# Kernel optimization log

Hardware: AMD Instinct MI355X
Metric: run time of the kernel (lower is better)

The kernel has to match this reference:

```python
import jax, jax.numpy as jnp
import numpy as np
from jax import lax

S = 30      # num_sensors
FD = 200    # feature_dim
T = 1024    # signal length
B = 1024    # batch
NC = 7      # num_classes


def setup_inputs() -> dict:
    key = jax.random.key(0)
    ks = jax.random.split(key, 24)
    rn = lambda i, shape: jax.random.normal(ks[i], shape, jnp.float32) * 0.05
    # normalized adjacency with self-loops: D^-1/2 (A+I) D^-1/2
    rng = np.random.default_rng(0)
    A = (rng.random((S, S)) > 0.7).astype(np.float32)
    A = ((A + A.T) > 0).astype(np.float32)
    A_self = A + np.eye(S, dtype=np.float32)
    dinv = 1.0 / np.sqrt(A_self.sum(1))
    adj_self = jnp.asarray(dinv[:, None] * A_self * dinv[None, :])
    return dict(
        x=jax.random.normal(ks[0], (B, S, T), jnp.float32),
        adj_self=adj_self,
        Wc1=rn(1, (S, S, 3)), bc1=jnp.zeros((S,), jnp.float32),
        Wc2=rn(2, (S, S, 3)), bc2=jnp.zeros((S,), jnp.float32),
        Wt=rn(3, (T, FD)), bt=jnp.zeros((FD,), jnp.float32),
        Wa=rn(4, (FD, FD)),
        Wm1=rn(5, (FD, FD)), Wm2=rn(6, (FD, FD)), Wm3=rn(7, (FD, FD)),
        Wg1=rn(8, (FD, FD)), Wg2=rn(9, (FD, FD)),
        wg=rn(10, (FD, 3)),
        Wp1=rn(11, (FD, FD // 2)), Wp2=rn(12, (FD, FD // 2)), Wp3=rn(13, (FD, FD // 2)),
        Wl=rn(14, (FD, 150)), Wgl=rn(15, (FD, 150)),
        Ws1=rn(16, (S, S // 2)), Ws2=rn(17, (S // 2, S)),
        Wf1=rn(18, (300, 150)), Wf2=rn(19, (150, 300)),
        Wcls=rn(20, (S * 600, NC)), bcls=jnp.zeros((NC,), jnp.float32),
    )


def reference(x, adj_self, Wc1, bc1, Wc2, bc2, Wt, bt, Wa, Wm1, Wm2, Wm3,
              Wg1, Wg2, wg, Wp1, Wp2, Wp3, Wl, Wgl, Ws1, Ws2, Wf1, Wf2,
              Wcls, bcls):
    dn = ('NCH', 'OIH', 'NCH')
    # CNN feature extractor: [B,S,T] -> [B,S,FD]
    h = jax.nn.relu(lax.conv_general_dilated(x, Wc1, (1,), 'SAME', dimension_numbers=dn) + bc1[None, :, None])
    h = jax.nn.relu(lax.conv_general_dilated(h, Wc2, (1,), 'SAME', dimension_numbers=dn) + bc2[None, :, None])
    F2 = jax.nn.relu(jnp.einsum('bst,tf->bsf', h, Wt) + bt)
    # MGCN: learned feature adjacency + 3-order GCN (batched, replaces per-sample loop)
    A_F = jax.nn.softmax(jax.nn.relu(jnp.einsum('bif,fg,bjg->bij', F2, Wa, F2)), axis=-1)
    gc = lambda A, X, W: jax.nn.relu(jnp.einsum('bij,bjf,fg->big', A, X, W))
    x1 = gc(A_F, F2, Wm1)
    x2 = gc(A_F, x1, Wm2)
    x3 = gc(A_F, x2, Wm3)
    # signal GCN on physical adjacency (2-layer, eval mode so dropout is identity)
    h1 = jax.nn.relu(jnp.einsum('ij,bjf,fg->big', adj_self, F2, Wg1))
    x_sensor = jnp.einsum('ij,bjf,fg->big', adj_self, h1, Wg2)
    H1 = (x1 + x_sensor) * 0.5
    H2 = (x2 + x_sensor) * 0.5
    H3 = (x3 + x_sensor) * 0.5
    # adaptive aggregation: per-node softmax gate over 3 branches, project to FD//2 each -> 300
    scores = jnp.stack([jnp.einsum('bsf,f->bs', H, wg[:, k]) for k, H in enumerate((H1, H2, H3))], -1)
    g = jax.nn.softmax(scores, -1)  # [B,S,3]
    agg = lambda k, H, Wp: jnp.einsum('ij,bjf,fg->big', adj_self, g[..., k:k + 1] * H, Wp)
    G_h = jnp.concatenate([agg(0, H1, Wp1), agg(1, H2, Wp2), agg(2, H3, Wp3)], -1)  # [B,S,300]
    # LGFM: local (physical adj) + global (learned adj) -> 150+150
    loc = jax.nn.relu(jnp.einsum('ij,bjf,fg->big', adj_self, F2, Wl))
    glb = jax.nn.relu(jnp.einsum('bij,bjf,fg->big', A_F, F2, Wgl))
    G_v = jnp.concatenate([loc, glb], -1)  # [B,S,300]
    # cross squeeze-excitation: channel SE on G_h driven by G_v, feature SE on G_v driven by G_h
    wch = jax.nn.sigmoid(jax.nn.relu(G_v.mean(-1) @ Ws1) @ Ws2)   # [B,S]
    G_h_att = G_h * wch[:, :, None]
    wft = jax.nn.sigmoid(jax.nn.relu(G_h.mean(1) @ Wf1) @ Wf2)    # [B,300]
    G_v_att = G_v * wft[:, None, :]
    G = jnp.concatenate([G_h_att, G_v_att], -1).reshape(x.shape[0], -1)  # [B, S*600]
    return jax.nn.log_softmax(G @ Wcls + bcls, axis=-1)
```

## Files before the change

kernel.cpp:

```cpp
#include <hip/hip_runtime.h>
#include <math.h>

#define S   30
#define FD  200
#define TT  1024
#define BB  1024
#define NC  7

#define OFS_C1   0ull
#define OFS_F2   31457280ull
#define OFS_AF   0ull
#define OFS_GV   921600ull
#define OFS_GH   10137600ull
#define OFS_WCH  19353600ull
#define OFS_WFT  19384320ull
#define OFS_R    19691520ull

__global__ __launch_bounds__(256) void k_conv1(
    const float* __restrict__ x,
    const float* __restrict__ Wc1, const float* __restrict__ bc1,
    float* __restrict__ C1) {
    const int c = blockIdx.x, b = blockIdx.y;
    const int t = threadIdx.x;
    const int t0 = c * 256;
    __shared__ float xb[S * 258];
    __shared__ float w1l[90 * 32];
    for (int idx = t; idx < 2700; idx += 256) {
        int so = idx / 90, r = idx % 90;
        w1l[r * 32 + so] = Wc1[idx];
    }
    for (int idx = t; idx < 180; idx += 256) {
        int r = idx >> 1, z = idx & 1;
        w1l[r * 32 + 30 + z] = 0.f;
    }
    for (int idx = t; idx < S * 64; idx += 256) {
        int s = idx >> 6, u = idx & 63;
        float4 v = *(const float4*)(x + (size_t)(b * S + s) * TT + t0 + 4 * u);
        float* d = xb + s * 258 + 1 + 4 * u;
        d[0] = v.x; d[1] = v.y; d[2] = v.z; d[3] = v.w;
    }
    if (t < 60) {
        int s = t % S;
        if (t < S) {
            int gt = t0 - 1;
            xb[s * 258] = (gt >= 0) ? x[(size_t)(b * S + s) * TT + gt] : 0.f;
        } else {
            int gt = t0 + 256;
            xb[s * 258 + 257] = (gt < TT) ? x[(size_t)(b * S + s) * TT + gt] : 0.f;
        }
    }
    __syncthreads();
    float acc[32];
#pragma unroll
    for (int so = 0; so < 32; so++) acc[so] = (so < S) ? bc1[so] : 0.f;
    for (int si = 0; si < S; si++) {
        float v0 = xb[si * 258 + t];
        float v1 = xb[si * 258 + t + 1];
        float v2 = xb[si * 258 + t + 2];
        const float* wr = w1l + si * 96;
#pragma unroll
        for (int u = 0; u < 8; u++) {
            float4 w0 = *(const float4*)(wr + 4 * u);
            float4 w1 = *(const float4*)(wr + 32 + 4 * u);
            float4 w2 = *(const float4*)(wr + 64 + 4 * u);
            acc[4 * u + 0] = fmaf(w0.x, v0, fmaf(w1.x, v1, fmaf(w2.x, v2, acc[4 * u + 0])));
            acc[4 * u + 1] = fmaf(w0.y, v0, fmaf(w1.y, v1, fmaf(w2.y, v2, acc[4 * u + 1])));
            acc[4 * u + 2] = fmaf(w0.z, v0, fmaf(w1.z, v1, fmaf(w2.z, v2, acc[4 * u + 2])));
            acc[4 * u + 3] = fmaf(w0.w, v0, fmaf(w1.w, v1, fmaf(w2.w, v2, acc[4 * u + 3])));
        }
    }
#pragma unroll
    for (int so = 0; so < 32; so++) {
        if (so < S)
            C1[(size_t)(b * S + so) * TT + t0 + t] = fmaxf(acc[so], 0.f);
    }
}

#define FMA4(av, wv, accm)                           \
    {                                                \
        accm[0] = fmaf(av, (wv).x, accm[0]);         \
        accm[1] = fmaf(av, (wv).y, accm[1]);         \
        accm[2] = fmaf(av, (wv).z, accm[2]);         \
        accm[3] = fmaf(av, (wv).w, accm[3]);         \
    }

__device__ inline void fma_tile8(const float4 a0, const float4 a1,
                                 const float4 w[8], float accm[4]) {
    FMA4(a0.x, w[0], accm); FMA4(a0.y, w[1], accm);
    FMA4(a0.z, w[2], accm); FMA4(a0.w, w[3], accm);
    FMA4(a1.x, w[4], accm); FMA4(a1.y, w[5], accm);
    FMA4(a1.z, w[6], accm); FMA4(a1.w, w[7], accm);
}

template<int RPT>
__device__ inline void zacc(float acc[][4]) {
#pragma unroll
    for (int m = 0; m < RPT; m++)
#pragma unroll
        for (int q = 0; q < 4; q++) acc[m][q] = 0.f;
}

template<int RPT, int N, int K>
__device__ inline void gemm_w4_pf(const float* Xl, int xstr, const float* __restrict__ W,
                                  int ct, int rt, float acc[][4]) {
    const float* wp = W + 4 * ct;
    float4 wreg[8];
#pragma unroll
    for (int u = 0; u < 8; u++) wreg[u] = *(const float4*)(wp + u * N);
#pragma unroll 1
    for (int kt = 0; kt < K / 8 - 1; kt++) {
        float4 wnxt[8];
#pragma unroll
        for (int u = 0; u < 8; u++) wnxt[u] = *(const float4*)(wp + (kt * 8 + 8 + u) * N);
#pragma unroll
        for (int m = 0; m < RPT; m++) {
            const float* xr = Xl + (rt * RPT + m) * xstr + kt * 8;
            float4 a0 = *(const float4*)(xr);
            float4 a1 = *(const float4*)(xr + 4);
            fma_tile8(a0, a1, wreg, acc[m]);
        }
#pragma unroll
        for (int u = 0; u < 8; u++) wreg[u] = wnxt[u];
    }
    {
        const int kb = K - 8;
#pragma unroll
        for (int m = 0; m < RPT; m++) {
            const float* xr = Xl + (rt * RPT + m) * xstr + kb;
            float4 a0 = *(const float4*)(xr);
            float4 a1 = *(const float4*)(xr + 4);
            fma_tile8(a0, a1, wreg, acc[m]);
        }
    }
}

template<int RPT, int N, int K>
__device__ inline void gemm_w4_pf_dual(const float* X0, const float* X1, int xstr,
                                       const float* __restrict__ W,
                                       int ct, int rt,
                                       float acc0[][4], float acc1[][4]) {
    const float* wp = W + 4 * ct;
    float4 wreg[8];
#pragma unroll
    for (int u = 0; u < 8; u++) wreg[u] = *(const float4*)(wp + u * N);
#pragma unroll 1
    for (int kt = 0; kt < K / 8 - 1; kt++) {
        float4 wnxt[8];
#pragma unroll
        for (int u = 0; u < 8; u++) wnxt[u] = *(const float4*)(wp + (kt * 8 + 8 + u) * N);
#pragma unroll
        for (int m = 0; m < RPT; m++) {
            const float* xr = X0 + (rt * RPT + m) * xstr + kt * 8;
            float4 a0 = *(const float4*)(xr);
            float4 a1 = *(const float4*)(xr + 4);
            fma_tile8(a0, a1, wreg, acc0[m]);
        }
#pragma unroll
        for (int m = 0; m < RPT; m++) {
            const float* xr = X1 + (rt * RPT + m) * xstr + kt * 8;
            float4 a0 = *(const float4*)(xr);
            float4 a1 = *(const float4*)(xr + 4);
            fma_tile8(a0, a1, wreg, acc1[m]);
        }
#pragma unroll
        for (int u = 0; u < 8; u++) wreg[u] = wnxt[u];
    }
    {
        const int kb = K - 8;
#pragma unroll
        for (int m = 0; m < RPT; m++) {
            const float* xr = X0 + (rt * RPT + m) * xstr + kb;
            float4 a0 = *(const float4*)(xr);
            float4 a1 = *(const float4*)(xr + 4);
            fma_tile8(a0, a1, wreg, acc0[m]);
        }
#pragma unroll
        for (int m = 0; m < RPT; m++) {
            const float* xr = X1 + (rt * RPT + m) * xstr + kb;
            float4 a0 = *(const float4*)(xr);
            float4 a1 = *(const float4*)(xr + 4);
            fma_tile8(a0, a1, wreg, acc1[m]);
        }
    }
}

template<int RPT>
__device__ inline void gemm_a32(const float* Al, const float* Xl, int xstr,
                                int ct, int rt, float acc[][4]) {
#pragma unroll
    for (int k4 = 0; k4 < 8; k4++) {
        float4 xv0 = *(const float4*)(Xl + (4 * k4 + 0) * xstr + 4 * ct);
        float4 xv1 = *(const float4*)(Xl + (4 * k4 + 1) * xstr + 4 * ct);
        float4 xv2 = *(const float4*)(Xl + (4 * k4 + 2) * xstr + 4 * ct);
        float4 xv3 = *(const float4*)(Xl + (4 * k4 + 3) * xstr + 4 * ct);
#pragma unroll
        for (int m = 0; m < RPT; m++) {
            float4 av = *(const float4*)(Al + (rt * RPT + m) * 32 + 4 * k4);
            FMA4(av.x, xv0, acc[m]);
            FMA4(av.y, xv1, acc[m]);
            FMA4(av.z, xv2, acc[m]);
            FMA4(av.w, xv3, acc[m]);
        }
    }
}

template<int RPT>
__device__ inline void gemm_a32_dual(const float* Al0, const float* X0,
                                     const float* Al1, const float* X1,
                                     int xstr, int ct, int rt,
                                     float acc0[][4], float acc1[][4]) {
#pragma unroll
    for (int k4 = 0; k4 < 8; k4++) {
        float4 x00 = *(const float4*)(X0 + (4 * k4 + 0) * xstr + 4 * ct);
        float4 x01 = *(const float4*)(X0 + (4 * k4 + 1) * xstr + 4 * ct);
        float4 x02 = *(const float4*)(X0 + (4 * k4 + 2) * xstr + 4 * ct);
        float4 x03 = *(const float4*)(X0 + (4 * k4 + 3) * xstr + 4 * ct);
        float4 x10 = *(const float4*)(X1 + (4 * k4 + 0) * xstr + 4 * ct);
        float4 x11 = *(const float4*)(X1 + (4 * k4 + 1) * xstr + 4 * ct);
        float4 x12 = *(const float4*)(X1 + (4 * k4 + 2) * xstr + 4 * ct);
        float4 x13 = *(const float4*)(X1 + (4 * k4 + 3) * xstr + 4 * ct);
#pragma unroll
        for (int m = 0; m < RPT; m++) {
            float4 av0 = *(const float4*)(Al0 + (rt * RPT + m) * 32 + 4 * k4);
            FMA4(av0.x, x00, acc0[m]);
            FMA4(av0.y, x01, acc0[m]);
            FMA4(av0.z, x02, acc0[m]);
            FMA4(av0.w, x03, acc0[m]);
            float4 av1 = *(const float4*)(Al1 + (rt * RPT + m) * 32 + 4 * k4);
            FMA4(av1.x, x10, acc1[m]);
            FMA4(av1.y, x11, acc1[m]);
            FMA4(av1.z, x12, acc1[m]);
            FMA4(av1.w, x13, acc1[m]);
        }
    }
}

__device__ inline void gemm_w150_pf(const float* Xl, const float* __restrict__ W,
                                    int ct2, int rt2, float acc[5][4], int off23) {
    const float* wp = W + 4 * ct2;
    float2 wa[8], wb[8];
#pragma unroll
    for (int u = 0; u < 8; u++) {
        wa[u] = *(const float2*)(wp + u * 150);
        wb[u] = *(const float2*)(wp + u * 150 + off23);
    }
#pragma unroll 1
    for (int kt = 0; kt < 24; kt++) {
        float2 na[8], nb[8];
#pragma unroll
        for (int u = 0; u < 8; u++) {
            int k = kt * 8 + 8 + u;
            na[u] = *(const float2*)(wp + k * 150);
            nb[u] = *(const float2*)(wp + k * 150 + off23);
        }
#pragma unroll
        for (int m = 0; m < 5; m++) {
            const float* xr = Xl + (rt2 * 5 + m) * FD + kt * 8;
            float4 a0 = *(const float4*)(xr);
            float4 a1 = *(const float4*)(xr + 4);
            float av[8] = {a0.x, a0.y, a0.z, a0.w, a1.x, a1.y, a1.z, a1.w};
#pragma unroll
            for (int u = 0; u < 8; u++) {
                acc[m][0] = fmaf(av[u], wa[u].x, acc[m][0]);
                acc[m][1] = fmaf(av[u], wa[u].y, acc[m][1]);
                acc[m][2] = fmaf(av[u], wb[u].x, acc[m][2]);
                acc[m][3] = fmaf(av[u], wb[u].y, acc[m][3]);
            }
        }
#pragma unroll
        for (int u = 0; u < 8; u++) { wa[u] = na[u]; wb[u] = nb[u]; }
    }
#pragma unroll
    for (int m = 0; m < 5; m++) {
        const float* xr = Xl + (rt2 * 5 + m) * FD + 192;
        float4 a0 = *(const float4*)(xr);
        float4 a1 = *(const float4*)(xr + 4);
        float av[8] = {a0.x, a0.y, a0.z, a0.w, a1.x, a1.y, a1.z, a1.w};
#pragma unroll
        for (int u = 0; u < 8; u++) {
            acc[m][0] = fmaf(av[u], wa[u].x, acc[m][0]);
            acc[m][1] = fmaf(av[u], wa[u].y, acc[m][1]);
            acc[m][2] = fmaf(av[u], wb[u].x, acc[m][2]);
            acc[m][3] = fmaf(av[u], wb[u].y, acc[m][3]);
        }
    }
}

__global__ __launch_bounds__(256) void k_f2(
    const float* __restrict__ C1,
    const float* __restrict__ Wc2, const float* __restrict__ bc2,
    const float* __restrict__ Wt, const float* __restrict__ bt,
    float* __restrict__ F2) {
    const int b = blockIdx.x, t = threadIdx.x;
    __shared__ float buf[S * 130];
    __shared__ float w2l[90 * 32];
    const int ct = t % 50, rt = t / 50;
    const int c3p = t & 63, sg = t >> 6;
    const int p0 = 2 * c3p;

    for (int idx = t; idx < 2700; idx += 256) {
        int ch = idx / 90, r = idx % 90;
        w2l[r * 32 + ch] = Wc2[idx];
    }
    for (int idx = t; idx < 180; idx += 256) {
        int r = idx >> 1, z = idx & 1;
        w2l[r * 32 + 30 + z] = 0.f;
    }
    float bias[8];
#pragma unroll
    for (int m = 0; m < 8; m++) {
        int ch = sg * 8 + m;
        bias[m] = bc2[ch < S ? ch : 0];
    }
    float acc[6][4];
    zacc<6>(acc);

    for (int ks = 0; ks < 8; ks++) {
        for (int idx = t; idx < S * 32; idx += 256) {
            int s = idx >> 5, u = idx & 31;
            float4 v = *(const float4*)(C1 + (size_t)(b * S + s) * TT + ks * 128 + 4 * u);
            float* d = buf + s * 130 + 1 + 4 * u;
            d[0] = v.x; d[1] = v.y; d[2] = v.z; d[3] = v.w;
        }
        if (t < 60) {
            int s = t % S;
            if (t < S) {
                int gt = ks * 128 - 1;
                buf[s * 130] = (gt >= 0) ? C1[(size_t)(b * S + s) * TT + gt] : 0.f;
            } else {
                int gt = ks * 128 + 128;
                buf[s * 130 + 129] = (gt < TT) ? C1[(size_t)(b * S + s) * TT + gt] : 0.f;
            }
        }
        __syncthreads();
        float a0[8], a1[8];
#pragma unroll
        for (int m = 0; m < 8; m++) { a0[m] = bias[m]; a1[m] = bias[m]; }
        for (int si = 0; si < S; si++) {
            float2 va = *(const float2*)(buf + si * 130 + p0);
            float2 vb = *(const float2*)(buf + si * 130 + p0 + 2);
            const float* wr = w2l + si * 96 + sg * 8;
            float4 w0a = *(const float4*)(wr);
            float4 w0b = *(const float4*)(wr + 4);
            float4 w1a = *(const float4*)(wr + 32);
            float4 w1b = *(const float4*)(wr + 36);
            float4 w2a = *(const float4*)(wr + 64);
            float4 w2b = *(const float4*)(wr + 68);
            float w0[8] = {w0a.x, w0a.y, w0a.z, w0a.w, w0b.x, w0b.y, w0b.z, w0b.w};
            float w1[8] = {w1a.x, w1a.y, w1a.z, w1a.w, w1b.x, w1b.y, w1b.z, w1b.w};
            float w2[8] = {w2a.x, w2a.y, w2a.z, w2a.w, w2b.x, w2b.y, w2b.z, w2b.w};
#pragma unroll
            for (int m = 0; m < 8; m++) {
                a0[m] = fmaf(w0[m], va.x, fmaf(w1[m], va.y, fmaf(w2[m], vb.x, a0[m])));
                a1[m] = fmaf(w0[m], va.y, fmaf(w1[m], vb.x, fmaf(w2[m], vb.y, a1[m])));
            }
        }
        __syncthreads();
#pragma unroll
        for (int m = 0; m < 8; m++) {
            int ch = sg * 8 + m;
            if (ch < S) {
                float2 o = {fmaxf(a0[m], 0.f), fmaxf(a1[m], 0.f)};
                *(float2*)(buf + ch * 128 + p0) = o;
            }
        }
        __syncthreads();
        if (t < 250)
            gemm_w4_pf<6, FD, 128>(buf, 128, Wt + (size_t)ks * 128 * FD, ct, rt, acc);
        __syncthreads();
    }
    if (t < 250) {
#pragma unroll
        for (int m = 0; m < 6; m++) {
            int row = rt * 6 + m;
            float4 o;
            o.x = fmaxf(acc[m][0] + bt[4 * ct + 0], 0.f);
            o.y = fmaxf(acc[m][1] + bt[4 * ct + 1], 0.f);
            o.z = fmaxf(acc[m][2] + bt[4 * ct + 2], 0.f);
            o.w = fmaxf(acc[m][3] + bt[4 * ct + 3], 0.f);
            *(float4*)(F2 + (size_t)(b * S + row) * FD + 4 * ct) = o;
        }
    }
}

__global__ __launch_bounds__(256) void k_att(
    const float* __restrict__ F2, const float* __restrict__ Wa,
    const float* __restrict__ adj, const float* __restrict__ Wl,
    const float* __restrict__ Wgl,
    float* __restrict__ AF, float* __restrict__ Gv) {
    const int b = blockIdx.x, t = threadIdx.x;
    __shared__ float A[32 * FD];
    __shared__ float Bu[32 * FD];
    __shared__ float scl[32 * 32];
    __shared__ float adjl[32 * 32];
    for (int idx = t; idx < 32 * FD; idx += 256) {
        A[idx] = (idx < S * FD) ? F2[(size_t)b * S * FD + idx] : 0.f;
        if (idx >= S * FD) Bu[idx] = 0.f;
    }
    for (int idx = t; idx < 1024; idx += 256) {
        int r = idx >> 5, cc = idx & 31;
        adjl[idx] = (r < S && cc < S) ? adj[r * S + cc] : 0.f;
        scl[idx] = 0.f;
    }
    __syncthreads();
    const int ct = t % 50, rt = t / 50;
    float acc[6][4];
    zacc<6>(acc);
    if (t < 250) {
        gemm_w4_pf<6, FD, FD>(A, FD, Wa, ct, rt, acc);
#pragma unroll
        for (int m = 0; m < 6; m++) {
            float4 o = {acc[m][0], acc[m][1], acc[m][2], acc[m][3]};
            *(float4*)(Bu + (rt * 6 + m) * FD + 4 * ct) = o;
        }
    }
    __syncthreads();
    for (int idx = t; idx < S * S; idx += 256) {
        int i = idx / S, j = idx % S;
        float a = 0.f;
        for (int f4 = 0; f4 < 50; f4++) {
            float4 p = *(const float4*)(Bu + i * FD + 4 * f4);
            float4 q = *(const float4*)(A + j * FD + 4 * f4);
            a = fmaf(p.x, q.x, a); a = fmaf(p.y, q.y, a);
            a = fmaf(p.z, q.z, a); a = fmaf(p.w, q.w, a);
        }
        scl[i * 32 + j] = fmaxf(a, 0.f);
    }
    __syncthreads();
    if (t < S) {
        float mx = -1e30f;
        for (int j = 0; j < S; j++) mx = fmaxf(mx, scl[t * 32 + j]);
        float den = 0.f;
        for (int j = 0; j < S; j++) den += expf(scl[t * 32 + j] - mx);
        float inv = 1.f / den;
        for (int j = 0; j < S; j++) scl[t * 32 + j] = expf(scl[t * 32 + j] - mx) * inv;
    }
    __syncthreads();
    for (int idx = t; idx < S * S; idx += 256)
        AF[(size_t)b * S * S + idx] = scl[(idx / S) * 32 + (idx % S)];
    zacc<6>(acc);
    if (t < 250) gemm_a32<6>(adjl, A, FD, ct, rt, acc);
    __syncthreads();
    if (t < 250)
#pragma unroll
        for (int m = 0; m < 6; m++) {
            float4 o = {acc[m][0], acc[m][1], acc[m][2], acc[m][3]};
            *(float4*)(Bu + (rt * 6 + m) * FD + 4 * ct) = o;
        }
    __syncthreads();
    const int ct2 = t % 38, rt2 = t / 38;
    const bool full = (4 * ct2 + 2) < 150;
    const int off23 = full ? 2 : -2;
    if (t < 228) {
        float a2[5][4];
        zacc<5>(a2);
        gemm_w150_pf(Bu, Wl, ct2, rt2, a2, off23);
#pragma unroll
        for (int m = 0; m < 5; m++) {
            float* o = Gv + (size_t)(b * S + rt2 * 5 + m) * 300 + 4 * ct2;
            o[0] = fmaxf(a2[m][0], 0.f); o[1] = fmaxf(a2[m][1], 0.f);
            if (full) { o[2] = fmaxf(a2[m][2], 0.f); o[3] = fmaxf(a2[m][3], 0.f); }
        }
    }
    __syncthreads();
    zacc<6>(acc);
    if (t < 250) gemm_a32<6>(scl, A, FD, ct, rt, acc);
    __syncthreads();
    if (t < 250)
#pragma unroll
        for (int m = 0; m < 6; m++) {
            float4 o = {acc[m][0], acc[m][1], acc[m][2], acc[m][3]};
            *(float4*)(Bu + (rt * 6 + m) * FD + 4 * ct) = o;
        }
    __syncthreads();
    if (t < 228) {
        float a2[5][4];
        zacc<5>(a2);
        gemm_w150_pf(Bu, Wgl, ct2, rt2, a2, off23);
#pragma unroll
        for (int m = 0; m < 5; m++) {
            float* o = Gv + (size_t)(b * S + rt2 * 5 + m) * 300 + 150 + 4 * ct2;
            o[0] = fmaxf(a2[m][0], 0.f); o[1] = fmaxf(a2[m][1], 0.f);
            if (full) { o[2] = fmaxf(a2[m][2], 0.f); o[3] = fmaxf(a2[m][3], 0.f); }
        }
    }
}

__global__ __launch_bounds__(256, 2) void k_mgcn(
    const float* __restrict__ F2g, const float* __restrict__ AFg,
    const float* __restrict__ adj,
    const float* __restrict__ Wg1, const float* __restrict__ Wg2,
    const float* __restrict__ Wm1, const float* __restrict__ Wm2,
    const float* __restrict__ Wm3, const float* __restrict__ wg,
    const float* __restrict__ Wp1, const float* __restrict__ Wp2,
    const float* __restrict__ Wp3,
    float* __restrict__ Rws, float* __restrict__ Gh) {
    const int b0 = blockIdx.x * 2, b1 = b0 + 1;
    const int t = threadIdx.x;
    __shared__ float A0[32 * FD], A1[32 * FD];
    __shared__ float afl0[1024], afl1[1024];
    __shared__ float adjl[1024];
    __shared__ float sk[192];
    __shared__ float gl[192];
    const int ct = t % 50, rt = t / 50;
    const int ct3 = t % 25, rt3 = t / 25;

    for (int idx = t; idx < 1500; idx += 256) {
        *(float4*)(A0 + 4 * idx) = *(const float4*)(F2g + (size_t)b0 * S * FD + 4 * idx);
        *(float4*)(A1 + 4 * idx) = *(const float4*)(F2g + (size_t)b1 * S * FD + 4 * idx);
    }
    for (int idx = t; idx < 400; idx += 256) { A0[6000 + idx] = 0.f; A1[6000 + idx] = 0.f; }
    for (int idx = t; idx < 1024; idx += 256) {
        int r = idx >> 5, cc = idx & 31;
        bool in = (r < S && cc < S);
        afl0[idx] = in ? AFg[(size_t)b0 * S * S + r * S + cc] : 0.f;
        afl1[idx] = in ? AFg[(size_t)b1 * S * S + r * S + cc] : 0.f;
        adjl[idx] = in ? adj[r * S + cc] : 0.f;
    }
    if (t < 192) sk[t] = 0.f;
    __syncthreads();

    float acc0[6][4], acc1[6][4], xsr0[6][4], xsr1[6][4];

#define DZ() { zacc<6>(acc0); zacc<6>(acc1); }
#define DWRITE(RELU)                                                        \
    if (t < 250) {                                                          \
        _Pragma("unroll")                                                   \
        for (int m = 0; m < 6; m++) {                                       \
            float4 o0, o1;                                                  \
            o0.x = RELU ? fmaxf(acc0[m][0], 0.f) : acc0[m][0];              \
            o0.y = RELU ? fmaxf(acc0[m][1], 0.f) : acc0[m][1];              \
            o0.z = RELU ? fmaxf(acc0[m][2], 0.f) : acc0[m][2];              \
            o0.w = RELU ? fmaxf(acc0[m][3], 0.f) : acc0[m][3];              \
            o1.x = RELU ? fmaxf(acc1[m][0], 0.f) : acc1[m][0];              \
            o1.y = RELU ? fmaxf(acc1[m][1], 0.f) : acc1[m][1];              \
            o1.z = RELU ? fmaxf(acc1[m][2], 0.f) : acc1[m][2];              \
            o1.w = RELU ? fmaxf(acc1[m][3], 0.f) : acc1[m][3];              \
            *(float4*)(A0 + (rt * 6 + m) * FD + 4 * ct) = o0;               \
            *(float4*)(A1 + (rt * 6 + m) * FD + 4 * ct) = o1;               \
        }                                                                   \
    }

    DZ();
    if (t < 250) gemm_a32_dual<6>(adjl, A0, adjl, A1, FD, ct, rt, acc0, acc1);
    __syncthreads();
    DWRITE(false);
    __syncthreads();
    DZ();
    if (t < 250) gemm_w4_pf_dual<6, FD, FD>(A0, A1, FD, Wg1, ct, rt, acc0, acc1);
    __syncthreads();
    DWRITE(true);
    __syncthreads();
    DZ();
    if (t < 250) gemm_a32_dual<6>(adjl, A0, adjl, A1, FD, ct, rt, acc0, acc1);
    __syncthreads();
    DWRITE(false);
    __syncthreads();
    DZ();
    if (t < 250) gemm_w4_pf_dual<6, FD, FD>(A0, A1, FD, Wg2, ct, rt, acc0, acc1);
    __syncthreads();
#pragma unroll
    for (int m = 0; m < 6; m++) {
#pragma unroll
        for (int q = 0; q < 4; q++) { xsr0[m][q] = acc0[m][q]; xsr1[m][q] = acc1[m][q]; }
    }
    for (int idx = t; idx < 1500; idx += 256) {
        *(float4*)(A0 + 4 * idx) = *(const float4*)(F2g + (size_t)b0 * S * FD + 4 * idx);
        *(float4*)(A1 + 4 * idx) = *(const float4*)(F2g + (size_t)b1 * S * FD + 4 * idx);
    }
    __syncthreads();

    const float* Wm[3] = {Wm1, Wm2, Wm3};
    const float* Wp[3] = {Wp1, Wp2, Wp3};
#pragma unroll 1
    for (int k = 0; k < 3; k++) {
        DZ();
        if (t < 250) gemm_a32_dual<6>(afl0, A0, afl1, A1, FD, ct, rt, acc0, acc1);
        __syncthreads();
        DWRITE(false);
        __syncthreads();
        DZ();
        if (t < 250) gemm_w4_pf_dual<6, FD, FD>(A0, A1, FD, Wm[k], ct, rt, acc0, acc1);
        __syncthreads();
        if (t < 250) {
#pragma unroll
            for (int m = 0; m < 6; m++) {
#pragma unroll
                for (int q = 0; q < 4; q++) {
                    acc0[m][q] = fmaxf(acc0[m][q], 0.f);
                    acc1[m][q] = fmaxf(acc1[m][q], 0.f);
                }
            }
#pragma unroll
            for (int m = 0; m < 6; m++) {
                int row = rt * 6 + m;
                float wg0 = wg[(4 * ct + 0) * 3 + k], wg1v = wg[(4 * ct + 1) * 3 + k];
                float wg2v = wg[(4 * ct + 2) * 3 + k], wg3 = wg[(4 * ct + 3) * 3 + k];
                float h00 = 0.5f * (acc0[m][0] + xsr0[m][0]);
                float h01 = 0.5f * (acc0[m][1] + xsr0[m][1]);
                float h02 = 0.5f * (acc0[m][2] + xsr0[m][2]);
                float h03 = 0.5f * (acc0[m][3] + xsr0[m][3]);
                float4 o0 = {h00, h01, h02, h03};
                *(float4*)(A0 + row * FD + 4 * ct) = o0;
                atomicAdd(&sk[row * 3 + k],
                          h00 * wg0 + h01 * wg1v + h02 * wg2v + h03 * wg3);
                float h10 = 0.5f * (acc1[m][0] + xsr1[m][0]);
                float h11 = 0.5f * (acc1[m][1] + xsr1[m][1]);
                float h12 = 0.5f * (acc1[m][2] + xsr1[m][2]);
                float h13 = 0.5f * (acc1[m][3] + xsr1[m][3]);
                float4 o1 = {h10, h11, h12, h13};
                *(float4*)(A1 + row * FD + 4 * ct) = o1;
                atomicAdd(&sk[96 + row * 3 + k],
                          h10 * wg0 + h11 * wg1v + h12 * wg2v + h13 * wg3);
            }
        }
        __syncthreads();
        if (t < 250) {
            float a30[3][4], a31[3][4];
            zacc<3>(a30); zacc<3>(a31);
            gemm_w4_pf_dual<3, 100, FD>(A0, A1, FD, Wp[k], ct3, rt3, a30, a31);
#pragma unroll
            for (int m = 0; m < 3; m++) {
                float4 o0 = {a30[m][0], a30[m][1], a30[m][2], a30[m][3]};
                float4 o1 = {a31[m][0], a31[m][1], a31[m][2], a31[m][3]};
                *(float4*)(Rws + ((size_t)(k * BB + b0) * S + rt3 * 3 + m) * 100 + 4 * ct3) = o0;
                *(float4*)(Rws + ((size_t)(k * BB + b1) * S + rt3 * 3 + m) * 100 + 4 * ct3) = o1;
            }
        }
        __syncthreads();
        if (k < 2) {
            DWRITE(false);
            __syncthreads();
        }
    }

    if (t < S) {
        float a0 = sk[t * 3 + 0], a1 = sk[t * 3 + 1], a2 = sk[t * 3 + 2];
        float m = fmaxf(a0, fmaxf(a1, a2));
        float e0 = expf(a0 - m), e1 = expf(a1 - m), e2 = expf(a2 - m);
        float inv = 1.f / (e0 + e1 + e2);
        gl[t * 3 + 0] = e0 * inv; gl[t * 3 + 1] = e1 * inv; gl[t * 3 + 2] = e2 * inv;
    } else if (t >= 64 && t < 64 + S) {
        int s = t - 64;
        float a0 = sk[96 + s * 3 + 0], a1 = sk[96 + s * 3 + 1], a2 = sk[96 + s * 3 + 2];
        float m = fmaxf(a0, fmaxf(a1, a2));
        float e0 = expf(a0 - m), e1 = expf(a1 - m), e2 = expf(a2 - m);
        float inv = 1.f / (e0 + e1 + e2);
        gl[96 + s * 3 + 0] = e0 * inv; gl[96 + s * 3 + 1] = e1 * inv; gl[96 + s * 3 + 2] = e2 * inv;
    }
    __syncthreads();

#pragma unroll 1
    for (int k = 0; k < 3; k++) {
        for (int idx = t; idx < S * 100; idx += 256) {
            int row = idx / 100, col = idx % 100;
            A0[row * FD + col] = Rws[((size_t)(k * BB + b0) * S) * 100 + idx];
            A1[row * FD + col] = Rws[((size_t)(k * BB + b1) * S) * 100 + idx];
        }
        for (int idx = t; idx < 1024; idx += 256) {
            int cc = idx & 31;
            afl0[idx] = (cc < S) ? adjl[idx] * gl[cc * 3 + k] : 0.f;
            afl1[idx] = (cc < S) ? adjl[idx] * gl[96 + cc * 3 + k] : 0.f;
        }
        __syncthreads();
        if (t < 250) {
            float a30[3][4], a31[3][4];
            zacc<3>(a30); zacc<3>(a31);
            gemm_a32_dual<3>(afl0, A0, afl1, A1, FD, ct3, rt3, a30, a31);
#pragma unroll
            for (int m = 0; m < 3; m++) {
                float4 o0 = {a30[m][0], a30[m][1], a30[m][2], a30[m][3]};
                float4 o1 = {a31[m][0], a31[m][1], a31[m][2], a31[m][3]};
                *(float4*)(Gh + (size_t)(b0 * S + rt3 * 3 + m) * 300 + k * 100 + 4 * ct3) = o0;
                *(float4*)(Gh + (size_t)(b1 * S + rt3 * 3 + m) * 300 + k * 100 + 4 * ct3) = o1;
            }
        }
        __syncthreads();
    }
#undef DZ
#undef DWRITE
}

__global__ __launch_bounds__(256) void k_se(const float* __restrict__ Gv, const float* __restrict__ Gh,
                                            const float* __restrict__ Ws1, const float* __restrict__ Ws2,
                                            const float* __restrict__ Wf1, const float* __restrict__ Wf2,
                                            float* __restrict__ wch, float* __restrict__ wft) {
    int b = blockIdx.x, t = threadIdx.x;
    __shared__ float mrow[S];
    __shared__ float u[15];
    __shared__ float mb[300];
    __shared__ float v[150];
    if (t < S) {
        float a = 0.f;
        const float* gp = Gv + ((size_t)b * S + t) * 300;
        for (int j = 0; j < 300; j++) a += gp[j];
        mrow[t] = a * (1.f / 300.f);
    }
    for (int j = t; j < 300; j += 256) {
        float a = 0.f;
        for (int s = 0; s < S; s++) a += Gh[(size_t)b * S * 300 + s * 300 + j];
        mb[j] = a * (1.f / S);
    }
    __syncthreads();
    if (t < 15) {
        float a = 0.f;
        for (int i = 0; i < S; i++) a += mrow[i] * Ws1[i * 15 + t];
        u[t] = fmaxf(a, 0.f);
    }
    if (t >= 64 && t < 64 + 150) {
        int h = t - 64;
        float a = 0.f;
        for (int j = 0; j < 300; j++) a += mb[j] * Wf1[j * 150 + h];
        v[h] = fmaxf(a, 0.f);
    }
    __syncthreads();
    if (t < S) {
        float a = 0.f;
        for (int h = 0; h < 15; h++) a += u[h] * Ws2[h * 30 + t];
        wch[b * S + t] = 1.f / (1.f + expf(-a));
    }
    for (int j = t; j < 300; j += 256) {
        float a = 0.f;
        for (int h = 0; h < 150; h++) a += v[h] * Wf2[h * 300 + j];
        wft[b * 300 + j] = 1.f / (1.f + expf(-a));
    }
}

__global__ __launch_bounds__(256) void k_cls(const float* __restrict__ Gh, const float* __restrict__ Gv,
                                             const float* __restrict__ wch, const float* __restrict__ wft,
                                             const float* __restrict__ Wcls, const float* __restrict__ bcls,
                                             float* __restrict__ out) {
    const int b = blockIdx.x, t = threadIdx.x;
    __shared__ float red[NC][256];
    __shared__ float wftl[300];
    __shared__ float wchl[S];
    for (int j = t; j < 300; j += 256) wftl[j] = wft[(size_t)b * 300 + j];
    if (t < S) wchl[t] = wch[b * S + t];
    __syncthreads();
    float acc[NC];
#pragma unroll
    for (int c = 0; c < NC; c++) acc[c] = 0.f;
    for (int i = t; i < S * 600; i += 256) {
        int s = i / 600, j = i % 600;
        float gval = (j < 300)
            ? Gh[(size_t)b * S * 300 + s * 300 + j] * wchl[s]
            : Gv[(size_t)b * S * 300 + s * 300 + (j - 300)] * wftl[j - 300];
        const float* wr = Wcls + (size_t)i * NC;
#pragma unroll
        for (int c = 0; c < NC; c++) acc[c] = fmaf(gval, wr[c], acc[c]);
    }
#pragma unroll
    for (int c = 0; c < NC; c++) red[c][t] = acc[c];
    __syncthreads();
    for (int off = 128; off > 0; off >>= 1) {
        if (t < off) {
#pragma unroll
            for (int c = 0; c < NC; c++) red[c][t] += red[c][t + off];
        }
        __syncthreads();
    }
    if (t == 0) {
        float lg[NC];
        float mx = -1e30f;
#pragma unroll
        for (int c = 0; c < NC; c++) { lg[c] = red[c][0] + bcls[c]; mx = fmaxf(mx, lg[c]); }
        float den = 0.f;
#pragma unroll
        for (int c = 0; c < NC; c++) den += expf(lg[c] - mx);
        float lden = logf(den) + mx;
#pragma unroll
        for (int c = 0; c < NC; c++) out[b * NC + c] = lg[c] - lden;
    }
}

extern "C" void kernel_launch(void* const* d_in, const int* in_sizes, int n_in,
                              void* d_out, int out_size, void* d_ws, size_t ws_size,
                              hipStream_t stream) {
    const float* x    = (const float*)d_in[0];
    const float* adj  = (const float*)d_in[1];
    const float* Wc1  = (const float*)d_in[2];
    const float* bc1  = (const float*)d_in[3];
    const float* Wc2  = (const float*)d_in[4];
    const float* bc2  = (const float*)d_in[5];
    const float* Wt   = (const float*)d_in[6];
    const float* bt   = (const float*)d_in[7];
    const float* Wa   = (const float*)d_in[8];
    const float* Wm1  = (const float*)d_in[9];
    const float* Wm2  = (const float*)d_in[10];
    const float* Wm3  = (const float*)d_in[11];
    const float* Wg1  = (const float*)d_in[12];
    const float* Wg2  = (const float*)d_in[13];
    const float* wg   = (const float*)d_in[14];
    const float* Wp1  = (const float*)d_in[15];
    const float* Wp2  = (const float*)d_in[16];
    const float* Wp3  = (const float*)d_in[17];
    const float* Wl   = (const float*)d_in[18];
    const float* Wgl  = (const float*)d_in[19];
    const float* Ws1  = (const float*)d_in[20];
    const float* Ws2  = (const float*)d_in[21];
    const float* Wf1  = (const float*)d_in[22];
    const float* Wf2  = (const float*)d_in[23];
    const float* Wcls = (const float*)d_in[24];
    const float* bcls = (const float*)d_in[25];

    float* ws  = (float*)d_ws;
    float* C1  = ws + OFS_C1;
    float* F2  = ws + OFS_F2;
    float* AF  = ws + OFS_AF;
    float* GV  = ws + OFS_GV;
    float* GH  = ws + OFS_GH;
    float* WCH = ws + OFS_WCH;
    float* WFT = ws + OFS_WFT;
    float* RWS = ws + OFS_R;
    float* out = (float*)d_out;

    k_conv1<<<dim3(4, BB), 256, 0, stream>>>(x, Wc1, bc1, C1);
    k_f2<<<BB, 256, 0, stream>>>(C1, Wc2, bc2, Wt, bt, F2);
    k_att<<<BB, 256, 0, stream>>>(F2, Wa, adj, Wl, Wgl, AF, GV);
    k_mgcn<<<BB / 2, 256, 0, stream>>>(F2, AF, adj, Wg1, Wg2, Wm1, Wm2, Wm3, wg,
                                       Wp1, Wp2, Wp3, RWS, GH);
    k_se<<<BB, 256, 0, stream>>>(GV, GH, Ws1, Ws2, Wf1, Wf2, WCH, WFT);
    k_cls<<<BB, 256, 0, stream>>>(GH, GV, WCH, WFT, Wcls, bcls, out);
}
```

Baseline: 1.145 ms.

## Fuse SE and classifier kernels and transpose Wcls for coalesced reads

Merges the squeeze-excitation kernel and the classifier kernel into one, so the per-batch channel and feature gate vectors stay in shared memory instead of going through global memory, and one launch disappears. A new small kernel transposes Wcls to class-major layout each call, so each class's weights are read contiguously across threads instead of with a stride of 7 floats. The cost is an extra transpose pass over the 126K-element weight every call and a larger workspace.

Result: no change. 1.147 ms (+0.2%).

```diff
diff --git a/kernel.cpp b/kernel.cpp
--- a/kernel.cpp
+++ b/kernel.cpp
@@ -12,9 +12,8 @@
 #define OFS_AF   0ull
 #define OFS_GV   921600ull
 #define OFS_GH   10137600ull
-#define OFS_WCH  19353600ull
-#define OFS_WFT  19384320ull
 #define OFS_R    19691520ull
+#define OFS_WT   28907520ull
 
 __global__ __launch_bounds__(256) void k_conv1(
     const float* __restrict__ x,
@@ -681,15 +680,29 @@
 #undef DWRITE
 }
 
-__global__ __launch_bounds__(256) void k_se(const float* __restrict__ Gv, const float* __restrict__ Gh,
-                                            const float* __restrict__ Ws1, const float* __restrict__ Ws2,
-                                            const float* __restrict__ Wf1, const float* __restrict__ Wf2,
-                                            float* __restrict__ wch, float* __restrict__ wft) {
-    int b = blockIdx.x, t = threadIdx.x;
+__global__ __launch_bounds__(256) void k_tw(const float* __restrict__ Wcls,
+                                            float* __restrict__ WclsT) {
+    int idx = blockIdx.x * 256 + threadIdx.x;
+    if (idx < S * 600 * NC) {
+        int i = idx / NC, c = idx % NC;
+        WclsT[c * (S * 600) + i] = Wcls[idx];
+    }
+}
+
+__global__ __launch_bounds__(256) void k_secls(
+    const float* __restrict__ Gh, const float* __restrict__ Gv,
+    const float* __restrict__ Ws1, const float* __restrict__ Ws2,
+    const float* __restrict__ Wf1, const float* __restrict__ Wf2,
+    const float* __restrict__ WclsT, const float* __restrict__ bcls,
+    float* __restrict__ out) {
+    const int b = blockIdx.x, t = threadIdx.x;
+    __shared__ float red[NC][256];
     __shared__ float mrow[S];
     __shared__ float u[15];
     __shared__ float mb[300];
     __shared__ float v[150];
+    __shared__ float wftl[300];
+    __shared__ float wchl[S];
     if (t < S) {
         float a = 0.f;
         const float* gp = Gv + ((size_t)b * S + t) * 300;
@@ -717,25 +730,13 @@
     if (t < S) {
         float a = 0.f;
         for (int h = 0; h < 15; h++) a += u[h] * Ws2[h * 30 + t];
-        wch[b * S + t] = 1.f / (1.f + expf(-a));
+        wchl[t] = 1.f / (1.f + expf(-a));
     }
     for (int j = t; j < 300; j += 256) {
         float a = 0.f;
         for (int h = 0; h < 150; h++) a += v[h] * Wf2[h * 300 + j];
-        wft[b * 300 + j] = 1.f / (1.f + expf(-a));
-    }
-}
-
-__global__ __launch_bounds__(256) void k_cls(const float* __restrict__ Gh, const float* __restrict__ Gv,
-                                             const float* __restrict__ wch, const float* __restrict__ wft,
-                                             const float* __restrict__ Wcls, const float* __restrict__ bcls,
-                                             float* __restrict__ out) {
-    const int b = blockIdx.x, t = threadIdx.x;
-    __shared__ float red[NC][256];
-    __shared__ float wftl[300];
-    __shared__ float wchl[S];
-    for (int j = t; j < 300; j += 256) wftl[j] = wft[(size_t)b * 300 + j];
-    if (t < S) wchl[t] = wch[b * S + t];
+        wftl[j] = 1.f / (1.f + expf(-a));
+    }
     __syncthreads();
     float acc[NC];
 #pragma unroll
@@ -745,9 +746,9 @@
         float gval = (j < 300)
             ? Gh[(size_t)b * S * 300 + s * 300 + j] * wchl[s]
             : Gv[(size_t)b * S * 300 + s * 300 + (j - 300)] * wftl[j - 300];
-        const float* wr = Wcls + (size_t)i * NC;
-#pragma unroll
-        for (int c = 0; c < NC; c++) acc[c] = fmaf(gval, wr[c], acc[c]);
+#pragma unroll
+        for (int c = 0; c < NC; c++)
+            acc[c] = fmaf(gval, WclsT[c * (S * 600) + i], acc[c]);
     }
 #pragma unroll
     for (int c = 0; c < NC; c++) red[c][t] = acc[c];
@@ -803,22 +804,21 @@
     const float* Wcls = (const float*)d_in[24];
     const float* bcls = (const float*)d_in[25];
 
-    float* ws  = (float*)d_ws;
-    float* C1  = ws + OFS_C1;
-    float* F2  = ws + OFS_F2;
-    float* AF  = ws + OFS_AF;
-    float* GV  = ws + OFS_GV;
-    float* GH  = ws + OFS_GH;
-    float* WCH = ws + OFS_WCH;
-    float* WFT = ws + OFS_WFT;
-    float* RWS = ws + OFS_R;
-    float* out = (float*)d_out;
+    float* ws    = (float*)d_ws;
+    float* C1    = ws + OFS_C1;
+    float* F2    = ws + OFS_F2;
+    float* AF    = ws + OFS_AF;
+    float* GV    = ws + OFS_GV;
+    float* GH    = ws + OFS_GH;
+    float* RWS   = ws + OFS_R;
+    float* WCLST = ws + OFS_WT;
+    float* out   = (float*)d_out;
 
     k_conv1<<<dim3(4, BB), 256, 0, stream>>>(x, Wc1, bc1, C1);
     k_f2<<<BB, 256, 0, stream>>>(C1, Wc2, bc2, Wt, bt, F2);
+    k_tw<<<(S * 600 * NC + 255) / 256, 256, 0, stream>>>(Wcls, WCLST);
     k_att<<<BB, 256, 0, stream>>>(F2, Wa, adj, Wl, Wgl, AF, GV);
     k_mgcn<<<BB / 2, 256, 0, stream>>>(F2, AF, adj, Wg1, Wg2, Wm1, Wm2, Wm3, wg,
                                        Wp1, Wp2, Wp3, RWS, GH);
-    k_se<<<BB, 256, 0, stream>>>(GV, GH, Ws1, Ws2, Wf1, Wf2, WCH, WFT);
-    k_cls<<<BB, 256, 0, stream>>>(GH, GV, WCH, WFT, Wcls, bcls, out);
-}
+    k_secls<<<BB, 256, 0, stream>>>(GH, GV, Ws1, Ws2, Wf1, Wf2, WCLST, bcls, out);
+}
```
